# Optimization experiments

Hardware: AMD Instinct MI355X
Metric: run time of the kernel (lower is better)

## Reference

```python
import jax, jax.numpy as jnp
import numpy as np
import math

NWIN = (16, 16)   # windows per side
P = 8             # win_patch
STRIDE = 4        # shift
H = 8             # num_head
HID = 128         # hidden_dim (per-head dim)
C = 128           # input_dim (== hidden_dim)
N = P * P         # tokens per window = 64
SDK = math.sqrt(HID)


def setup_inputs() -> dict:
    key = jax.random.key(0)
    ks = jax.random.split(key, 11)
    s = 0.02
    return {
        "x": jax.random.normal(ks[0], (NWIN[0] * NWIN[1] * 4, N, C), jnp.float32),
        "mask": jax.random.uniform(ks[1], (3, N, N), jnp.float32),
        "Bp": jax.random.normal(ks[2], (N, N), jnp.float32),
        "wq_w": jax.random.normal(ks[3], (H * HID, C), jnp.float32) * s,
        "wq_b": jax.random.normal(ks[4], (H * HID,), jnp.float32) * s,
        "wk_w": jax.random.normal(ks[5], (H * HID, C), jnp.float32) * s,
        "wk_b": jax.random.normal(ks[6], (H * HID,), jnp.float32) * s,
        "wv_w": jax.random.normal(ks[7], (H * HID, C), jnp.float32) * s,
        "wv_b": jax.random.normal(ks[8], (H * HID,), jnp.float32) * s,
        "proj_w": jax.random.normal(ks[9], (C, H * HID), jnp.float32) * s,
        "proj_b": jax.random.normal(ks[10], (C,), jnp.float32) * s,
    }


def reference(x, mask, Bp, wq_w, wq_b, wk_w, wk_b, wv_w, wv_b, proj_w, proj_b):
    nh, nw = NWIN
    b = x.shape[0] // (nh * nw)

    # windows -> full image, shift by (-stride, -stride), re-partition
    img = x.reshape(b, nh, nw, P, P, C).transpose(0, 1, 3, 2, 4, 5)
    img = img.reshape(b, nh * P, nw * P, C)
    img = jnp.roll(img, (-STRIDE, -STRIDE), axis=(1, 2))
    xw = img.reshape(b, nh, P, nw, P, C).transpose(0, 1, 3, 2, 4, 5).reshape(-1, N, C)

    q = xw @ wq_w.T + wq_b
    k = xw @ wk_w.T + wk_b
    v = xw @ wv_w.T + wv_b
    Bw = q.shape[0]  # total windows
    q = q.reshape(Bw, N, H, HID).transpose(0, 2, 1, 3)
    k = k.reshape(Bw, N, H, HID).transpose(0, 2, 1, 3)
    v = v.reshape(Bw, N, H, HID).transpose(0, 2, 1, 3)

    att = jnp.einsum("bhnd,bhmd->bhnm", q, k) / jnp.asarray(SDK, q.dtype) + Bp
    att = jax.nn.softmax(att, axis=-1)

    # border-window multiplicative mask (interior windows pass through)
    att = att.reshape(b, nh, nw, H, N, N)
    wmask = jnp.ones((nh, nw, 1, N, N), dtype=att.dtype)
    wmask = wmask.at[-1, :-1].set(mask[0])   # bottom row (except corner)
    wmask = wmask.at[:-1, -1].set(mask[1])   # right column (except corner)
    wmask = wmask.at[-1, -1].set(mask[2])    # bottom-right corner
    att = (att * wmask[None]).reshape(Bw, H, N, N)

    out = jnp.einsum("bhnm,bhmd->bhnd", att, v)
    out = out.transpose(0, 2, 1, 3).reshape(Bw, N, H * HID)
    out = out @ proj_w.T + proj_b

    # reverse shift and re-partition into windows
    img = out.reshape(b, nh, nw, P, P, C).transpose(0, 1, 3, 2, 4, 5)
    img = img.reshape(b, nh * P, nw * P, C)
    img = jnp.roll(img, (STRIDE, STRIDE), axis=(1, 2))
    return img.reshape(b, nh, P, nw, P, C).transpose(0, 1, 3, 2, 4, 5).reshape(-1, N, C)
```

## Files before the change

kernel.cpp:

```cpp
#include <hip/hip_runtime.h>
#include <hip/hip_bf16.h>

typedef __attribute__((ext_vector_type(8))) short bf16x8;
typedef __attribute__((ext_vector_type(4))) float f32x4;

#define LXW  0
#define LT   16384
#define LV   32768
#define LRW  49152

__device__ __forceinline__ int sw256(int o){ return o ^ (((o >> 8) & 7) << 4); }
__device__ __forceinline__ int sw128(int o){ return o ^ (((o >> 7) & 7) << 4); }

__device__ __forceinline__ short f2bf(float f){
  union { float f; unsigned u; } v; v.f = f;
  unsigned r = v.u + 0x7FFFu + ((v.u >> 16) & 1u);
  return (short)(r >> 16);
}
__device__ __forceinline__ float bf2f(short s){
  union { unsigned u; float f; } v; v.u = ((unsigned)(unsigned short)s) << 16;
  return v.f;
}
__device__ __forceinline__ bf16x8 lds8(const char* smem, int off){
  return *(const bf16x8*)(smem + off);
}

__global__ void wfused_k(const float* __restrict__ pw, const float* __restrict__ wv,
                         const float* __restrict__ wv_b,
                         short* __restrict__ wf, float* __restrict__ bf) {
  int blk = blockIdx.x;
  int h = blk >> 7, co = blk & 127;
  int ci = threadIdx.x;
  const float* pr = pw + (size_t)co * 1024 + h * 128;
  const float* wr = wv + (size_t)h * 128 * 128 + ci;
  float acc = 0.f;
#pragma unroll 4
  for (int d = 0; d < 128; ++d)
    acc += pr[d] * wr[(size_t)d * 128];
  wf[(size_t)h * 16384 + co * 128 + ci] = f2bf(acc);
  if (ci < 64) {
    float b = wv_b[h*128 + ci] * pr[ci] + wv_b[h*128 + 64 + ci] * pr[64 + ci];
    b += __shfl_xor(b, 1);  b += __shfl_xor(b, 2);  b += __shfl_xor(b, 4);
    b += __shfl_xor(b, 8);  b += __shfl_xor(b, 16); b += __shfl_xor(b, 32);
    if (ci == 0) bf[h*128 + co] = b;
  }
}

__global__ void mt_k(const float* __restrict__ wq, const float* __restrict__ wk,
                     const float* __restrict__ bq, const float* __restrict__ bk,
                     short* __restrict__ mt, float* __restrict__ uarr,
                     float* __restrict__ varr, float* __restrict__ carr) {
  const float isdk = 0.088388347648318447f;
  int blk = blockIdx.x;
  int h = blk >> 7, kp = blk & 127;
  int ci = threadIdx.x;
  const float* wkc = wk + (size_t)h * 16384 + kp;
  const float* wqc = wq + (size_t)h * 16384 + ci;
  float macc = 0.f, vacc = 0.f;
#pragma unroll 4
  for (int d = 0; d < 128; ++d) {
    float wqv = wqc[(size_t)d * 128];
    macc += wkc[(size_t)d * 128] * wqv;
    vacc += bk[h*128 + d] * wqv;
  }
  mt[(size_t)h * 16384 + kp * 128 + ci] = f2bf(macc * isdk);
  if (ci == 0) {
    float u = 0.f;
#pragma unroll 4
    for (int d = 0; d < 128; ++d) u += bq[h*128 + d] * wkc[(size_t)d * 128];
    uarr[h*128 + kp] = u * isdk;
  }
  if (kp == 0) {
    varr[h*128 + ci] = vacc * isdk;
    if (ci == 0) {
      float c = 0.f;
#pragma unroll 4
      for (int d = 0; d < 128; ++d) c += bq[h*128 + d] * bk[h*128 + d];
      carr[h] = c * isdk;
    }
  }
}

__global__ __launch_bounds__(256) void swattn_main(
    const float* __restrict__ x, const float* __restrict__ mask,
    const float* __restrict__ Bp, const float* __restrict__ proj_b,
    const short* __restrict__ mt, const short* __restrict__ wfz,
    const float* __restrict__ uarr, const float* __restrict__ bfu,
    const float* __restrict__ varr, const float* __restrict__ carr,
    float* __restrict__ out)
{
  __shared__ alignas(16) char smem[51200];
  const int tid  = threadIdx.x;
  const int wvid = tid >> 6, lane = tid & 63, lr = lane & 15, lg = lane >> 4;
  const int rbp  = (wvid >> 1) * 2;
  const int jh   = wvid & 1;
  const int wid = blockIdx.x;
  const int bb = wid >> 8, wy = (wid >> 4) & 15, wx = wid & 15;

  {
    int token = tid >> 2, q = tid & 3;
    int py = token >> 3, px = token & 7;
    int Y = (wy*8 + py + 4) & 127;
    int X = (wx*8 + px + 4) & 127;
    int swin = bb*256 + ((Y>>3)<<4) + (X>>3);
    int stok = ((Y&7)<<3) + (X&7);
    const float* src = x + ((size_t)(swin*64 + stok))*128 + q*32;
    int base = LXW + token*256 + q*64;
#pragma unroll
    for (int j = 0; j < 32; j += 8) {
      float4 f0 = *(const float4*)(src + j);
      float4 f1 = *(const float4*)(src + j + 4);
      bf16x8 bv;
      bv[0]=f2bf(f0.x); bv[1]=f2bf(f0.y); bv[2]=f2bf(f0.z); bv[3]=f2bf(f0.w);
      bv[4]=f2bf(f1.x); bv[5]=f2bf(f1.y); bv[6]=f2bf(f1.z); bv[7]=f2bf(f1.w);
      *(bf16x8*)(smem + sw256(base + j*2)) = bv;
    }
  }
  __syncthreads();

  bf16x8 af[2][4];
#pragma unroll
  for (int r2 = 0; r2 < 2; ++r2) {
    int arow = (rbp + r2)*16 + lr;
#pragma unroll
    for (int kk = 0; kk < 4; ++kk)
      af[r2][kk] = *(const bf16x8*)(smem + sw256(LXW + arow*256 + kk*64 + lg*16));
  }

#pragma unroll
  for (int e2 = 0; e2 < 2; ++e2) {
    int e = tid*2 + e2;
    int h = e >> 6, i = e & 63;
    float acc = carr[h];
#pragma unroll
    for (int k8 = 0; k8 < 16; ++k8) {
      bf16x8 xv = lds8(smem, sw256(LXW + i*256 + k8*16));
      float4 va = *(const float4*)(varr + h*128 + k8*8);
      float4 vb = *(const float4*)(varr + h*128 + k8*8 + 4);
      acc += bf2f(xv[0])*va.x + bf2f(xv[1])*va.y + bf2f(xv[2])*va.z + bf2f(xv[3])*va.w;
      acc += bf2f(xv[4])*vb.x + bf2f(xv[5])*vb.y + bf2f(xv[6])*vb.z + bf2f(xv[7])*vb.w;
    }
    *(float*)(smem + LRW + e*4) = acc;
  }
  __syncthreads();

  const float* mrow = nullptr;
  if (wy == 15 && wx != 15)      mrow = mask;
  else if (wx == 15 && wy != 15) mrow = mask + 4096;
  else if (wy == 15 && wx == 15) mrow = mask + 8192;

  f32x4 accO[8];
#pragma unroll
  for (int ct = 0; ct < 8; ++ct) accO[ct] = f32x4{0.f, 0.f, 0.f, 0.f};

  for (int h = 0; h < 8; ++h) {
    {
      const short* wmat[2] = { mt, wfz };
      const float* bvec[2] = { uarr, bfu };
#pragma unroll
      for (int s = 0; s < 2; ++s) {
#pragma unroll
        for (int t = 0; t < 4; ++t) {
          int j = (jh*4 + t)*16 + lr;
          const short* wr = wmat[s] + (size_t)(h*128 + j)*128;
          bf16x8 bfv[4];
#pragma unroll
          for (int kk = 0; kk < 4; ++kk)
            bfv[kk] = *(const bf16x8*)(wr + kk*32 + lg*8);
          float bias = bvec[s][h*128 + j];
#pragma unroll
          for (int r2 = 0; r2 < 2; ++r2) {
            int rb = rbp + r2;
            f32x4 acc = f32x4{0.f,0.f,0.f,0.f};
#pragma unroll
            for (int kk = 0; kk < 4; ++kk)
              acc = __builtin_amdgcn_mfma_f32_16x16x32_bf16(af[r2][kk], bfv[kk], acc, 0,0,0);
            if (s == 0) {
#pragma unroll
              for (int rr = 0; rr < 4; ++rr) {
                int row = rb*16 + lg*4 + rr;
                *(short*)(smem + sw256(LT + row*256 + j*2)) = f2bf(acc[rr] + bias);
              }
            } else {
              short4 p;
              p.x = f2bf(acc[0] + bias); p.y = f2bf(acc[1] + bias);
              p.z = f2bf(acc[2] + bias); p.w = f2bf(acc[3] + bias);
              int m0 = rb*16 + lg*4;
              *(short4*)(smem + sw128(LV + j*128 + m0*2)) = p;
            }
          }
        }
      }
    }
    __syncthreads();

    {
      float pv[4][4];
      bf16x8 qf[4];
      int qrow = 16*wvid + lr;
#pragma unroll
      for (int kk = 0; kk < 4; ++kk)
        qf[kk] = *(const bf16x8*)(smem + sw256(LT + qrow*256 + kk*64 + lg*16));
      int i0 = 16*wvid + lg*4;
      float rwb[4];
#pragma unroll
      for (int rr = 0; rr < 4; ++rr)
        rwb[rr] = *(const float*)(smem + LRW + (h*64 + i0 + rr)*4);
      __builtin_amdgcn_s_setprio(1);
#pragma unroll
      for (int cb = 0; cb < 4; ++cb) {
        f32x4 at = f32x4{0.f,0.f,0.f,0.f};
        int krow = cb*16 + lr;
#pragma unroll
        for (int kk = 0; kk < 4; ++kk) {
          bf16x8 kf = *(const bf16x8*)(smem + sw256(LXW + krow*256 + kk*64 + lg*16));
          at = __builtin_amdgcn_mfma_f32_16x16x32_bf16(qf[kk], kf, at, 0,0,0);
        }
#pragma unroll
        for (int rr = 0; rr < 4; ++rr)
          pv[cb][rr] = at[rr] + rwb[rr] + Bp[(i0+rr)*64 + cb*16 + lr];
      }
      __builtin_amdgcn_s_setprio(0);
#pragma unroll
      for (int rr = 0; rr < 4; ++rr) {
        float s = 0.f;
#pragma unroll
        for (int cb = 0; cb < 4; ++cb) { pv[cb][rr] = __expf(pv[cb][rr]); s += pv[cb][rr]; }
        s += __shfl_xor(s, 1); s += __shfl_xor(s, 2);
        s += __shfl_xor(s, 4); s += __shfl_xor(s, 8);
        float inv = 1.0f / s;
#pragma unroll
        for (int cb = 0; cb < 4; ++cb) pv[cb][rr] *= inv;
      }
      if (mrow) {
#pragma unroll
        for (int cb = 0; cb < 4; ++cb)
#pragma unroll
          for (int rr = 0; rr < 4; ++rr)
            pv[cb][rr] *= mrow[(i0+rr)*64 + cb*16 + lr];
      }
#pragma unroll
      for (int cb = 0; cb < 4; ++cb) {
        int mcol = cb*16 + lr;
#pragma unroll
        for (int rr = 0; rr < 4; ++rr)
          *(short*)(smem + sw256(LT + (i0+rr)*256 + mcol*2)) = f2bf(pv[cb][rr]);
      }
    }

    {
      bf16x8 paf[2];
#pragma unroll
      for (int kk = 0; kk < 2; ++kk)
        paf[kk] = lds8(smem, sw256(LT + (16*wvid + lr)*256 + kk*64 + lg*16));
      __builtin_amdgcn_s_setprio(1);
#pragma unroll
      for (int ct = 0; ct < 8; ++ct) {
        int d = ct*16 + lr;
#pragma unroll
        for (int kk = 0; kk < 2; ++kk) {
          bf16x8 vf = lds8(smem, sw128(LV + d*128 + kk*64 + lg*16));
          accO[ct] = __builtin_amdgcn_mfma_f32_16x16x32_bf16(paf[kk], vf, accO[ct], 0,0,0);
        }
      }
      __builtin_amdgcn_s_setprio(0);
    }
    __syncthreads();
  }

#pragma unroll
  for (int rr = 0; rr < 4; ++rr) {
    int i = 16*wvid + lg*4 + rr;
    int py = i >> 3, px = i & 7;
    int Y = (wy*8 + py + 4) & 127;
    int X = (wx*8 + px + 4) & 127;
    int dwin = bb*256 + ((Y>>3)<<4) + (X>>3);
    int dtok = ((Y&7)<<3) + (X&7);
    float* dst = out + ((size_t)(dwin*64 + dtok))*128;
#pragma unroll
    for (int ct = 0; ct < 8; ++ct)
      dst[ct*16 + lr] = accO[ct][rr] + proj_b[ct*16 + lr];
  }
}

extern "C" void kernel_launch(void* const* d_in, const int* in_sizes, int n_in,
                              void* d_out, int out_size, void* d_ws, size_t ws_size,
                              hipStream_t stream) {
  (void)in_sizes; (void)n_in; (void)out_size; (void)ws_size;
  const float* x      = (const float*)d_in[0];
  const float* mask   = (const float*)d_in[1];
  const float* Bp     = (const float*)d_in[2];
  const float* wq_w   = (const float*)d_in[3];
  const float* wq_b   = (const float*)d_in[4];
  const float* wk_w   = (const float*)d_in[5];
  const float* wk_b   = (const float*)d_in[6];
  const float* wv_w   = (const float*)d_in[7];
  const float* wv_b   = (const float*)d_in[8];
  const float* proj_w = (const float*)d_in[9];
  const float* proj_b = (const float*)d_in[10];
  float* out = (float*)d_out;
  short* wsb  = (short*)d_ws;
  short* wfz  = wsb;
  short* mt   = wsb + 131072;
  float* bfu  = (float*)(wsb + 262144);
  float* uarr = bfu + 1024;
  float* varr = bfu + 2048;
  float* carr = bfu + 3072;

  wfused_k<<<1024, 128, 0, stream>>>(proj_w, wv_w, wv_b, wfz, bfu);
  mt_k<<<1024, 128, 0, stream>>>(wq_w, wk_w, wq_b, wk_b, mt, uarr, varr, carr);
  swattn_main<<<1024, 256, 0, stream>>>(x, mask, Bp, proj_b,
      mt, wfz, uarr, bfu, varr, carr, out);
}
```

Before: 194.0 us.

## Cache window token fragments in registers and drop LDS copy of input

Each wave now loads the MFMA fragments for all 64 tokens of the shifted window into registers once, instead of keeping a separate LDS buffer for the input. Those register fragments serve both as the A operand of the Q/V projections and as the key operand of the QK^T MFMAs. The q·k loop is reordered to stream Q fragments against four independent accumulators. This cuts shared memory per block from about 50KB to 34KB, which could allow more resident blocks per CU, and removes repeated per-head LDS reads of the input. The cost is roughly 32 more VGPRs per thread, which could offset the occupancy gain or cause spills.

```diff
diff --git a/kernel.cpp b/kernel.cpp
--- a/kernel.cpp
+++ b/kernel.cpp
@@ -4,10 +4,9 @@
 typedef __attribute__((ext_vector_type(8))) short bf16x8;
 typedef __attribute__((ext_vector_type(4))) float f32x4;
 
-#define LXW  0
-#define LT   16384
-#define LV   32768
-#define LRW  49152
+#define LT   0
+#define LV   16384
+#define LRW  32768
 
 __device__ __forceinline__ int sw256(int o){ return o ^ (((o >> 8) & 7) << 4); }
 __device__ __forceinline__ int sw128(int o){ return o ^ (((o >> 7) & 7) << 4); }
@@ -89,7 +88,7 @@
     const float* __restrict__ varr, const float* __restrict__ carr,
     float* __restrict__ out)
 {
-  __shared__ alignas(16) char smem[51200];
+  __shared__ alignas(16) char smem[34816];
   const int tid  = threadIdx.x;
   const int wvid = tid >> 6, lane = tid & 63, lr = lane & 15, lg = lane >> 4;
   const int rbp  = (wvid >> 1) * 2;
@@ -105,7 +104,7 @@
     int swin = bb*256 + ((Y>>3)<<4) + (X>>3);
     int stok = ((Y&7)<<3) + (X&7);
     const float* src = x + ((size_t)(swin*64 + stok))*128 + q*32;
-    int base = LXW + token*256 + q*64;
+    int base = LT + token*256 + q*64;
 #pragma unroll
     for (int j = 0; j < 32; j += 8) {
       float4 f0 = *(const float4*)(src + j);
@@ -118,14 +117,12 @@
   }
   __syncthreads();
 
-  bf16x8 af[2][4];
-#pragma unroll
-  for (int r2 = 0; r2 < 2; ++r2) {
-    int arow = (rbp + r2)*16 + lr;
+  bf16x8 kfr[4][4];
+#pragma unroll
+  for (int cb = 0; cb < 4; ++cb)
 #pragma unroll
     for (int kk = 0; kk < 4; ++kk)
-      af[r2][kk] = *(const bf16x8*)(smem + sw256(LXW + arow*256 + kk*64 + lg*16));
-  }
+      kfr[cb][kk] = lds8(smem, sw256(LT + (cb*16 + lr)*256 + kk*64 + lg*16));
 
 #pragma unroll
   for (int e2 = 0; e2 < 2; ++e2) {
@@ -134,7 +131,7 @@
     float acc = carr[h];
 #pragma unroll
     for (int k8 = 0; k8 < 16; ++k8) {
-      bf16x8 xv = lds8(smem, sw256(LXW + i*256 + k8*16));
+      bf16x8 xv = lds8(smem, sw256(LT + i*256 + k8*16));
       float4 va = *(const float4*)(varr + h*128 + k8*8);
       float4 vb = *(const float4*)(varr + h*128 + k8*8 + 4);
       acc += bf2f(xv[0])*va.x + bf2f(xv[1])*va.y + bf2f(xv[2])*va.z + bf2f(xv[3])*va.w;
@@ -174,7 +171,7 @@
             f32x4 acc = f32x4{0.f,0.f,0.f,0.f};
 #pragma unroll
             for (int kk = 0; kk < 4; ++kk)
-              acc = __builtin_amdgcn_mfma_f32_16x16x32_bf16(af[r2][kk], bfv[kk], acc, 0,0,0);
+              acc = __builtin_amdgcn_mfma_f32_16x16x32_bf16(kfr[rb][kk], bfv[kk], acc, 0,0,0);
             if (s == 0) {
 #pragma unroll
               for (int rr = 0; rr < 4; ++rr) {
@@ -196,31 +193,29 @@
 
     {
       float pv[4][4];
-      bf16x8 qf[4];
+      f32x4 at[4];
+#pragma unroll
+      for (int cb = 0; cb < 4; ++cb) at[cb] = f32x4{0.f,0.f,0.f,0.f};
       int qrow = 16*wvid + lr;
-#pragma unroll
-      for (int kk = 0; kk < 4; ++kk)
-        qf[kk] = *(const bf16x8*)(smem + sw256(LT + qrow*256 + kk*64 + lg*16));
+      __builtin_amdgcn_s_setprio(1);
+#pragma unroll
+      for (int kk = 0; kk < 4; ++kk) {
+        bf16x8 qfk = lds8(smem, sw256(LT + qrow*256 + kk*64 + lg*16));
+#pragma unroll
+        for (int cb = 0; cb < 4; ++cb)
+          at[cb] = __builtin_amdgcn_mfma_f32_16x16x32_bf16(qfk, kfr[cb][kk], at[cb], 0,0,0);
+      }
+      __builtin_amdgcn_s_setprio(0);
       int i0 = 16*wvid + lg*4;
       float rwb[4];
 #pragma unroll
       for (int rr = 0; rr < 4; ++rr)
         rwb[rr] = *(const float*)(smem + LRW + (h*64 + i0 + rr)*4);
-      __builtin_amdgcn_s_setprio(1);
-#pragma unroll
-      for (int cb = 0; cb < 4; ++cb) {
-        f32x4 at = f32x4{0.f,0.f,0.f,0.f};
-        int krow = cb*16 + lr;
-#pragma unroll
-        for (int kk = 0; kk < 4; ++kk) {
-          bf16x8 kf = *(const bf16x8*)(smem + sw256(LXW + krow*256 + kk*64 + lg*16));
-          at = __builtin_amdgcn_mfma_f32_16x16x32_bf16(qf[kk], kf, at, 0,0,0);
-        }
+#pragma unroll
+      for (int cb = 0; cb < 4; ++cb)
 #pragma unroll
         for (int rr = 0; rr < 4; ++rr)
-          pv[cb][rr] = at[rr] + rwb[rr] + Bp[(i0+rr)*64 + cb*16 + lr];
-      }
-      __builtin_amdgcn_s_setprio(0);
+          pv[cb][rr] = at[cb][rr] + rwb[rr] + Bp[(i0+rr)*64 + cb*16 + lr];
 #pragma unroll
       for (int rr = 0; rr < 4; ++rr) {
         float s = 0.f;
```

Measured after the change: 272.7 us. +40.6%, slower.
